# Kernel tuning notes

Measured on AMD Instinct MI355X. Metric: run time of the kernel, lower is better.

The kernel has to match this reference:

```python
import jax, jax.numpy as jnp
import numpy as np

H, K, D = 4096, 16, 256  # hidden_dim, num_slots, slot_dim
BOT = 512                # decoder bottleneck
N_ITER = 3
EPS = 1e-5


def _ln(x, g, b):
    mu = jnp.mean(x, axis=-1, keepdims=True)
    var = jnp.var(x, axis=-1, keepdims=True)
    return (x - mu) * jax.lax.rsqrt(var + EPS) * g + b


def setup_inputs() -> dict:
    key = jax.random.key(0)
    ks = jax.random.split(key, 24)
    r = lambda i, shape, s=0.02: jax.random.normal(ks[i], shape, jnp.float32) * s
    inp = {
        "hidden_states": jax.random.normal(ks[0], (8, 4096, H), jnp.float32),
        "old_slots": jax.random.normal(ks[1], (8, K, D), jnp.float32) * 0.02,
        # SlotAttention params
        "in_w": r(2, (H, D)), "in_b": jnp.zeros((D,), jnp.float32),
        "ln_in_g": jnp.ones((D,), jnp.float32), "ln_in_b": jnp.zeros((D,), jnp.float32),
        "ln_s_g": jnp.ones((D,), jnp.float32), "ln_s_b": jnp.zeros((D,), jnp.float32),
        "ln_m_g": jnp.ones((D,), jnp.float32), "ln_m_b": jnp.zeros((D,), jnp.float32),
        "q_w": r(3, (D, D)), "k_w": r(4, (D, D)), "v_w": r(5, (D, D)),
        "mlp_w1": r(6, (D, 2 * D)), "mlp_b1": jnp.zeros((2 * D,), jnp.float32),
        "mlp_w2": r(7, (2 * D, D)), "mlp_b2": jnp.zeros((D,), jnp.float32),
        # ReconstructionDecoder params
        "dec_w1": r(8, (D, BOT)), "dec_b1": jnp.zeros((BOT,), jnp.float32),
        "dec_w2": r(9, (BOT, BOT)), "dec_b2": jnp.zeros((BOT,), jnp.float32),
        "dec_w3": r(10, (BOT, H)), "dec_b3": jnp.zeros((H,), jnp.float32),
    }
    return inp


def _forward(hidden_states, old_slots, in_w, in_b, ln_in_g, ln_in_b, ln_s_g, ln_s_b,
             ln_m_g, ln_m_b, q_w, k_w, v_w, mlp_w1, mlp_b1, mlp_w2, mlp_b2,
             dec_w1, dec_b1, dec_w2, dec_b2, dec_w3, dec_b3):
    B, T, _ = hidden_states.shape
    # subsample: 256 linspace over front + last 256 tokens (T > 512 branch)
    idx_front = jnp.linspace(0.0, T - 256, 256).astype(jnp.int32)  # torch long cast truncates; values are exact floor here
    idx_back = jnp.arange(T - 256, T, dtype=jnp.int32)
    idx = jnp.concatenate([idx_front, idx_back])
    sampled = hidden_states[:, idx, :]                 # [B, 512, H]

    x = _ln(sampled @ in_w + in_b, ln_in_g, ln_in_b)   # [B, 512, D]
    k = x @ k_w                                        # [B, 512, D]
    v = x @ v_w
    scale = D ** (-0.5)

    slots = old_slots                                  # [B, K, D]
    for _ in range(N_ITER):
        s = _ln(slots, ln_s_g, ln_s_b)
        q = s @ q_w
        logits = jnp.einsum('bkd,bnd->bkn', q, k) * scale
        attn = jax.nn.softmax(logits, axis=1)          # softmax over SLOT axis
        upd = jnp.einsum('bkn,bnd->bkd', attn, v)
        h = _ln(upd, ln_m_g, ln_m_b)
        slots = s + jax.nn.gelu(h @ mlp_w1 + mlp_b1, approximate=False) @ mlp_w2 + mlp_b2

    # reconstruction loss
    target = jax.lax.stop_gradient(jnp.mean(hidden_states, axis=1))     # [B, H]
    r = jax.nn.gelu(slots @ dec_w1 + dec_b1, approximate=False)
    r = jax.nn.gelu(r @ dec_w2 + dec_b2, approximate=False)
    r = r @ dec_w3 + dec_b3                                             # [B, K, H]
    recon = jnp.mean(r, axis=1)                                         # [B, H]
    recon_loss = jnp.mean((recon - target) ** 2)
    return slots, recon_loss


def reference(hidden_states, old_slots, in_w, in_b, ln_in_g, ln_in_b, ln_s_g, ln_s_b,
              ln_m_g, ln_m_b, q_w, k_w, v_w, mlp_w1, mlp_b1, mlp_w2, mlp_b2,
              dec_w1, dec_b1, dec_w2, dec_b2, dec_w3, dec_b3):
    return _forward(hidden_states, old_slots, in_w, in_b, ln_in_g, ln_in_b, ln_s_g,
                    ln_s_b, ln_m_g, ln_m_b, q_w, k_w, v_w, mlp_w1, mlp_b1, mlp_w2,
                    mlp_b2, dec_w1, dec_b1, dec_w2, dec_b2, dec_w3, dec_b3)
```

## Files before the change

kernel.cpp:

```cpp
#include <hip/hip_runtime.h>

typedef unsigned short u16;
typedef float f32x4 __attribute__((ext_vector_type(4)));
typedef __bf16 bf16x8 __attribute__((ext_vector_type(8)));
typedef u16 u16x4 __attribute__((ext_vector_type(4)));

__device__ __forceinline__ u16 f2bf(float f){
  __bf16 h = (__bf16)f;
  union { __bf16 h; u16 u; } x; x.h = h;
  return x.u;
}
__device__ __forceinline__ float bf2f(u16 s){
  union { unsigned u; float f; } x; x.u = ((unsigned)s) << 16;
  return x.f;
}
__device__ __forceinline__ f32x4 mfma16(bf16x8 a, bf16x8 b, f32x4 c){
  return __builtin_amdgcn_mfma_f32_16x16x32_bf16(a, b, c, 0, 0, 0);
}
__device__ __forceinline__ float wred_sum(float x){
  #pragma unroll
  for (int m = 1; m < 64; m <<= 1) x += __shfl_xor(x, m);
  return x;
}
__device__ __forceinline__ float gelu_f(float v){
  return 0.5f * v * (1.0f + erff(v * 0.70710678118654752440f));
}
__device__ __forceinline__ int sample_idx(int r){
  return (r < 256) ? (3840 * r) / 255 : (3584 + r);
}

__global__ __launch_bounds__(256) void k_prep(
    const float* __restrict__ in_w, const float* __restrict__ q_w,
    const float* __restrict__ k_w, const float* __restrict__ v_w,
    const float* __restrict__ w1, const float* __restrict__ w2,
    u16* __restrict__ in_wT, u16* __restrict__ q_wT, u16* __restrict__ k_wT,
    u16* __restrict__ v_wT, u16* __restrict__ w1T, u16* __restrict__ w2T,
    float* __restrict__ loss_slot)
{
  __shared__ float tile[64][65];
  int id = blockIdx.x;
  const float* src; u16* dst; int R, C, t;
  if (id < 256)      { src=in_w; dst=in_wT; R=4096; C=256; t=id; }
  else if (id < 272) { src=q_w;  dst=q_wT;  R=256;  C=256; t=id-256; }
  else if (id < 288) { src=k_w;  dst=k_wT;  R=256;  C=256; t=id-272; }
  else if (id < 304) { src=v_w;  dst=v_wT;  R=256;  C=256; t=id-288; }
  else if (id < 336) { src=w1;   dst=w1T;   R=256;  C=512; t=id-304; }
  else               { src=w2;   dst=w2T;   R=512;  C=256; t=id-336; }
  int tC = C >> 6;
  int r0 = (t / tC) * 64, c0 = (t % tC) * 64;
  int tr = threadIdx.x >> 6, tc = threadIdx.x & 63;
  #pragma unroll
  for (int rr = tr; rr < 64; rr += 4)
    tile[rr][tc] = src[(size_t)(r0+rr)*C + c0 + tc];
  __syncthreads();
  #pragma unroll
  for (int cc = tr; cc < 64; cc += 4)
    dst[(size_t)(c0+cc)*R + r0 + tc] = f2bf(tile[tc][cc]);
  if (id == 0 && threadIdx.x == 0) *loss_slot = 0.f;
}

__global__ __launch_bounds__(256) void k_colsum(const float* __restrict__ hs,
                                                float* __restrict__ parts)
{
  int tc = blockIdx.x;
  int hb = blockIdx.y;
  int b  = blockIdx.z;
  int h0 = hb*1024 + threadIdx.x*4;
  const float* p = hs + ((size_t)b*4096 + (size_t)tc*64)*4096 + h0;
  f32x4 s = {0.f,0.f,0.f,0.f};
  for (int t = 0; t < 64; ++t)
    s += *reinterpret_cast<const f32x4*>(p + (size_t)t*4096);
  *reinterpret_cast<f32x4*>(parts + ((size_t)(b*64+tc) << 12) + h0) = s;
}

__global__ __launch_bounds__(256) void k_colsum2(const float* __restrict__ parts,
                                                 float* __restrict__ tgt)
{
  int i = blockIdx.x*256 + threadIdx.x;
  int b = i >> 12, h = i & 4095;
  float s = 0.f;
  for (int c = 0; c < 64; ++c) s += parts[((size_t)(b*64+c) << 12) + h];
  tgt[i] = s * (1.0f/4096.0f);
}

__global__ __launch_bounds__(512) void k_in_gemm_ln(
    const float* __restrict__ hs, const u16* __restrict__ in_wT,
    const float* __restrict__ in_b,
    const float* __restrict__ ln_g, const float* __restrict__ ln_b,
    u16* __restrict__ x_b)
{
  __shared__ float xt[16][260];
  const int lane = threadIdx.x & 63;
  const int w = threadIdx.x >> 6;
  const int c16 = lane & 15, g4 = lane >> 4;
  const int m0 = blockIdx.x * 16;
  const int row = m0 + c16;
  const int b = row >> 9;
  const int tok = row & 511;
  const int src = sample_idx(tok);
  const float* arow = hs + ((size_t)b*4096 + src)*4096 + g4*8;

  f32x4 acc[2];
  acc[0] = (f32x4){0.f,0.f,0.f,0.f};
  acc[1] = (f32x4){0.f,0.f,0.f,0.f};

  for (int k0 = 0; k0 < 4096; k0 += 32) {
    f32x4 a0 = *reinterpret_cast<const f32x4*>(arow + k0);
    f32x4 a1 = *reinterpret_cast<const f32x4*>(arow + k0 + 4);
    union { u16 u[8]; bf16x8 v; } af;
    #pragma unroll
    for (int i=0;i<4;++i){ af.u[i] = f2bf(a0[i]); af.u[4+i] = f2bf(a1[i]); }
    #pragma unroll
    for (int ct=0; ct<2; ++ct){
      int col = w*32 + ct*16 + c16;
      bf16x8 bf = *reinterpret_cast<const bf16x8*>(in_wT + (size_t)col*4096 + k0 + g4*8);
      acc[ct] = mfma16(af.v, bf, acc[ct]);
    }
  }
  #pragma unroll
  for (int ct=0; ct<2; ++ct){
    int col = w*32 + ct*16 + c16;
    float bias = in_b[col];
    #pragma unroll
    for (int i=0;i<4;++i) xt[g4*4+i][col] = acc[ct][i] + bias;
  }
  __syncthreads();
  #pragma unroll
  for (int rr=0; rr<2; ++rr){
    int r = 2*w + rr;
    f32x4 v = *reinterpret_cast<const f32x4*>(&xt[r][4*lane]);
    float s = v[0]+v[1]+v[2]+v[3];
    float q = v[0]*v[0]+v[1]*v[1]+v[2]*v[2]+v[3]*v[3];
    s = wred_sum(s); q = wred_sum(q);
    float mu = s*(1.0f/256.0f);
    float var = q*(1.0f/256.0f) - mu*mu;
    float rs = rsqrtf(var + 1e-5f);
    u16x4 pk;
    #pragma unroll
    for (int i=0;i<4;++i) pk[i] = f2bf((v[i]-mu)*rs*ln_g[4*lane+i] + ln_b[4*lane+i]);
    *reinterpret_cast<u16x4*>(x_b + (size_t)(m0 + r)*256 + 4*lane) = pk;
  }
}

__global__ __launch_bounds__(256) void k_kv(
    const u16* __restrict__ x_b, const u16* __restrict__ k_wT, const u16* __restrict__ v_wT,
    u16* __restrict__ k_out, u16* __restrict__ vT_out)
{
  const int lane = threadIdx.x & 63;
  const int w = threadIdx.x >> 6;
  const int c16 = lane & 15, g4 = lane >> 4;
  const int m0 = blockIdx.x * 16;
  const u16* aptr = x_b + (size_t)(m0 + c16)*256 + g4*8;
  f32x4 ak[4], av[4];
  #pragma unroll
  for (int ct=0; ct<4; ++ct){ ak[ct]=(f32x4){0.f,0.f,0.f,0.f}; av[ct]=(f32x4){0.f,0.f,0.f,0.f}; }
  #pragma unroll
  for (int kk=0; kk<8; ++kk){
    bf16x8 af = *reinterpret_cast<const bf16x8*>(aptr + kk*32);
    #pragma unroll
    for (int ct=0; ct<4; ++ct){
      int col = w*64 + ct*16 + c16;
      bf16x8 bk = *reinterpret_cast<const bf16x8*>(k_wT + (size_t)col*256 + kk*32 + g4*8);
      bf16x8 bv = *reinterpret_cast<const bf16x8*>(v_wT + (size_t)col*256 + kk*32 + g4*8);
      ak[ct] = mfma16(af, bk, ak[ct]);
      av[ct] = mfma16(af, bv, av[ct]);
    }
  }
  const int b = m0 >> 9;
  const int tok0 = (m0 & 511) + g4*4;
  #pragma unroll
  for (int ct=0; ct<4; ++ct){
    int col = w*64 + ct*16 + c16;
    #pragma unroll
    for (int i=0;i<4;++i)
      k_out[(size_t)(m0 + g4*4 + i)*256 + col] = f2bf(ak[ct][i]);
    u16x4 pk;
    #pragma unroll
    for (int i=0;i<4;++i) pk[i] = f2bf(av[ct][i]);
    *reinterpret_cast<u16x4*>(vT_out + ((size_t)(b*256 + col))*512 + tok0) = pk;
  }
}

__global__ __launch_bounds__(1024) void k_slots(
    const float* __restrict__ old_slots,
    const u16* __restrict__ k_b, const u16* __restrict__ vT_b,
    const u16* __restrict__ q_wT, const u16* __restrict__ w1T, const u16* __restrict__ w2T,
    const float* __restrict__ ln_s_g, const float* __restrict__ ln_s_b,
    const float* __restrict__ ln_m_g, const float* __restrict__ ln_m_b,
    const float* __restrict__ mlp_b1, const float* __restrict__ mlp_b2,
    float* __restrict__ out_slots)
{
  __shared__ u16 bufA[16*264];
  __shared__ u16 qS[16*264];
  __shared__ u16 wideS[16*520];
  __shared__ u16 updS[16*264];

  const int lane = threadIdx.x & 63;
  const int w    = threadIdx.x >> 6;
  const int c16  = lane & 15;
  const int g4   = lane >> 4;
  const int b    = blockIdx.x;

  const u16* kb = k_b  + (size_t)b * 512 * 256;
  const u16* vb = vT_b + (size_t)b * 256 * 512;

  float sl[4];
  {
    const float* p = old_slots + ((size_t)b*16 + w)*256 + 4*lane;
    #pragma unroll
    for (int i=0;i<4;++i) sl[i] = p[i];
  }
  float lsg[4], lsbv[4], lmg[4], lmb[4];
  #pragma unroll
  for (int i=0;i<4;++i){
    lsg[i]  = ln_s_g[4*lane+i];
    lsbv[i] = ln_s_b[4*lane+i];
    lmg[i]  = ln_m_g[4*lane+i];
    lmb[i]  = ln_m_b[4*lane+i];
  }
  const float b1a = mlp_b1[32*w + c16];
  const float b1b = mlp_b1[32*w + 16 + c16];
  const float b2c = mlp_b2[16*w + c16];
  float sv[4];

  for (int it = 0; it < 3; ++it) {
    {
      float s = sl[0]+sl[1]+sl[2]+sl[3];
      float q = sl[0]*sl[0]+sl[1]*sl[1]+sl[2]*sl[2]+sl[3]*sl[3];
      s = wred_sum(s); q = wred_sum(q);
      float mu = s * (1.0f/256.0f);
      float var = q * (1.0f/256.0f) - mu*mu;
      float rs = rsqrtf(var + 1e-5f);
      u16x4 pk;
      #pragma unroll
      for (int i=0;i<4;++i){ sv[i] = (sl[i]-mu)*rs*lsg[i] + lsbv[i]; pk[i] = f2bf(sv[i]); }
      *reinterpret_cast<u16x4*>(bufA + w*264 + 4*lane) = pk;
    }
    __syncthreads();

    {
      f32x4 acc = {0.f,0.f,0.f,0.f};
      #pragma unroll
      for (int kk = 0; kk < 8; ++kk) {
        bf16x8 af = *reinterpret_cast<const bf16x8*>(bufA + c16*264 + kk*32 + g4*8);
        bf16x8 bf = *reinterpret_cast<const bf16x8*>(q_wT + (size_t)(16*w + c16)*256 + kk*32 + g4*8);
        acc = mfma16(af, bf, acc);
      }
      #pragma unroll
      for (int i=0;i<4;++i) qS[(g4*4+i)*264 + 16*w + c16] = f2bf(acc[i]);
    }
    __syncthreads();

    {
      bf16x8 qf[8];
      #pragma unroll
      for (int kk=0;kk<8;++kk)
        qf[kk] = *reinterpret_cast<const bf16x8*>(qS + c16*264 + kk*32 + g4*8);
      #pragma unroll
      for (int ct=0; ct<2; ++ct) {
        int n0 = 32*w + 16*ct;
        f32x4 acc = {0.f,0.f,0.f,0.f};
        #pragma unroll
        for (int kk=0;kk<8;++kk){
          bf16x8 bf = *reinterpret_cast<const bf16x8*>(kb + (size_t)(n0 + c16)*256 + kk*32 + g4*8);
          acc = mfma16(qf[kk], bf, acc);
        }
        float t0 = acc[0]*0.0625f, t1 = acc[1]*0.0625f, t2 = acc[2]*0.0625f, t3 = acc[3]*0.0625f;
        float mx = fmaxf(fmaxf(t0,t1), fmaxf(t2,t3));
        mx = fmaxf(mx, __shfl_xor(mx,16));
        mx = fmaxf(mx, __shfl_xor(mx,32));
        float e0 = expf(t0-mx), e1 = expf(t1-mx), e2 = expf(t2-mx), e3 = expf(t3-mx);
        float ss = e0+e1+e2+e3;
        ss += __shfl_xor(ss,16);
        ss += __shfl_xor(ss,32);
        float inv = 1.0f/ss;
        wideS[(g4*4+0)*520 + n0 + c16] = f2bf(e0*inv);
        wideS[(g4*4+1)*520 + n0 + c16] = f2bf(e1*inv);
        wideS[(g4*4+2)*520 + n0 + c16] = f2bf(e2*inv);
        wideS[(g4*4+3)*520 + n0 + c16] = f2bf(e3*inv);
      }
    }
    __syncthreads();

    {
      f32x4 acc = {0.f,0.f,0.f,0.f};
      #pragma unroll
      for (int kk=0; kk<16; ++kk){
        bf16x8 af = *reinterpret_cast<const bf16x8*>(wideS + c16*520 + kk*32 + g4*8);
        bf16x8 bf = *reinterpret_cast<const bf16x8*>(vb + (size_t)(16*w + c16)*512 + kk*32 + g4*8);
        acc = mfma16(af, bf, acc);
      }
      #pragma unroll
      for (int i=0;i<4;++i) updS[(g4*4+i)*264 + 16*w + c16] = f2bf(acc[i]);
    }
    __syncthreads();

    {
      u16x4 up = *reinterpret_cast<const u16x4*>(updS + w*264 + 4*lane);
      float uv[4];
      #pragma unroll
      for (int i=0;i<4;++i) uv[i] = bf2f(up[i]);
      float s = uv[0]+uv[1]+uv[2]+uv[3];
      float q = uv[0]*uv[0]+uv[1]*uv[1]+uv[2]*uv[2]+uv[3]*uv[3];
      s = wred_sum(s); q = wred_sum(q);
      float mu = s*(1.0f/256.0f);
      float var = q*(1.0f/256.0f) - mu*mu;
      float rs = rsqrtf(var + 1e-5f);
      u16x4 pk;
      #pragma unroll
      for (int i=0;i<4;++i) pk[i] = f2bf((uv[i]-mu)*rs*lmg[i] + lmb[i]);
      *reinterpret_cast<u16x4*>(bufA + w*264 + 4*lane) = pk;
    }
    __syncthreads();

    {
      bf16x8 hf[8];
      #pragma unroll
      for (int kk=0;kk<8;++kk)
        hf[kk] = *reinterpret_cast<const bf16x8*>(bufA + c16*264 + kk*32 + g4*8);
      #pragma unroll
      for (int ct=0; ct<2; ++ct){
        int n0 = 32*w + 16*ct;
        float bb = ct ? b1b : b1a;
        f32x4 acc = {0.f,0.f,0.f,0.f};
        #pragma unroll
        for (int kk=0;kk<8;++kk){
          bf16x8 bf = *reinterpret_cast<const bf16x8*>(w1T + (size_t)(n0 + c16)*256 + kk*32 + g4*8);
          acc = mfma16(hf[kk], bf, acc);
        }
        #pragma unroll
        for (int i=0;i<4;++i)
          wideS[(g4*4+i)*520 + n0 + c16] = f2bf(gelu_f(acc[i] + bb));
      }
    }
    __syncthreads();

    {
      f32x4 acc = {0.f,0.f,0.f,0.f};
      #pragma unroll
      for (int kk=0; kk<16; ++kk){
        bf16x8 af = *reinterpret_cast<const bf16x8*>(wideS + c16*520 + kk*32 + g4*8);
        bf16x8 bf = *reinterpret_cast<const bf16x8*>(w2T + (size_t)(16*w + c16)*512 + kk*32 + g4*8);
        acc = mfma16(af, bf, acc);
      }
      #pragma unroll
      for (int i=0;i<4;++i) bufA[(g4*4+i)*264 + 16*w + c16] = f2bf(acc[i] + b2c);
    }
    __syncthreads();
    {
      u16x4 ns = *reinterpret_cast<const u16x4*>(bufA + w*264 + 4*lane);
      #pragma unroll
      for (int i=0;i<4;++i) sl[i] = sv[i] + bf2f(ns[i]);
    }
    __syncthreads();
  }

  {
    float* p = out_slots + ((size_t)b*16 + w)*256 + 4*lane;
    #pragma unroll
    for (int i=0;i<4;++i) p[i] = sl[i];
  }
}

__global__ __launch_bounds__(256) void k_dec(
    const float* __restrict__ slots, const float* __restrict__ w1, const float* __restrict__ b1,
    const float* __restrict__ w2, const float* __restrict__ b2, float* __restrict__ r2g)
{
  __shared__ float sr[256];
  __shared__ float r1[512];
  const int row = blockIdx.x;
  const int t = threadIdx.x;
  sr[t] = slots[(size_t)row*256 + t];
  __syncthreads();
  float a0 = b1[t], a1 = b1[t+256];
  for (int i=0;i<256;++i){
    float s = sr[i];
    a0 = fmaf(s, w1[(size_t)i*512 + t], a0);
    a1 = fmaf(s, w1[(size_t)i*512 + t + 256], a1);
  }
  r1[t] = gelu_f(a0); r1[t+256] = gelu_f(a1);
  __syncthreads();
  float c0 = b2[t], c1 = b2[t+256];
  for (int i=0;i<512;++i){
    float s = r1[i];
    c0 = fmaf(s, w2[(size_t)i*512 + t], c0);
    c1 = fmaf(s, w2[(size_t)i*512 + t + 256], c1);
  }
  r2g[(size_t)row*512 + t]       = gelu_f(c0);
  r2g[(size_t)row*512 + t + 256] = gelu_f(c1);
}

__global__ __launch_bounds__(256) void k_loss_part(
    const float* __restrict__ r2g, const float* __restrict__ w3, const float* __restrict__ b3,
    float* __restrict__ rpart)
{
  __shared__ float rb[128];
  const int hb = blockIdx.x;
  const int b  = blockIdx.y;
  const int jc = blockIdx.z;
  const int t  = threadIdx.x;
  const int j0 = jc*128;
  if (t < 128){
    float s = 0.f;
    #pragma unroll
    for (int k2=0;k2<16;++k2) s += r2g[(size_t)(b*16 + k2)*512 + j0 + t];
    rb[t] = s * (1.0f/16.0f);
  }
  __syncthreads();
  const int h = hb*1024 + t*4;
  f32x4 acc;
  if (jc == 0) acc = *reinterpret_cast<const f32x4*>(b3 + h);
  else         acc = (f32x4){0.f,0.f,0.f,0.f};
  for (int j=0;j<128;++j){
    f32x4 wv = *reinterpret_cast<const f32x4*>(w3 + (size_t)(j0+j)*4096 + h);
    float rj = rb[j];
    acc[0] = fmaf(rj, wv[0], acc[0]);
    acc[1] = fmaf(rj, wv[1], acc[1]);
    acc[2] = fmaf(rj, wv[2], acc[2]);
    acc[3] = fmaf(rj, wv[3], acc[3]);
  }
  *reinterpret_cast<f32x4*>(rpart + (((size_t)jc*8 + b) << 12) + h) = acc;
}

__global__ __launch_bounds__(256) void k_loss_final(
    const float* __restrict__ rpart, const float* __restrict__ tgt,
    float* __restrict__ loss)
{
  __shared__ float red[4];
  int i = blockIdx.x*256 + threadIdx.x;
  int b = i >> 12, h = i & 4095;
  float r = 0.f;
  #pragma unroll
  for (int jc=0; jc<4; ++jc) r += rpart[(((size_t)jc*8 + b) << 12) + h];
  float d = r - tgt[i];
  float loc = wred_sum(d*d);
  const int lane = threadIdx.x & 63, wv_ = threadIdx.x >> 6;
  if (lane == 0) red[wv_] = loc;
  __syncthreads();
  if (threadIdx.x == 0){
    float s = (red[0]+red[1]+red[2]+red[3]) * (1.0f/32768.0f);
    atomicAdd(loss, s);
  }
}

extern "C" void kernel_launch(void* const* d_in, const int* in_sizes, int n_in,
                              void* d_out, int out_size, void* d_ws, size_t ws_size,
                              hipStream_t stream)
{
  const float* hs      = (const float*)d_in[0];
  const float* oslots  = (const float*)d_in[1];
  const float* in_w    = (const float*)d_in[2];
  const float* in_b    = (const float*)d_in[3];
  const float* ln_in_g = (const float*)d_in[4];
  const float* ln_in_b = (const float*)d_in[5];
  const float* ln_s_g  = (const float*)d_in[6];
  const float* ln_s_b  = (const float*)d_in[7];
  const float* ln_m_g  = (const float*)d_in[8];
  const float* ln_m_b  = (const float*)d_in[9];
  const float* q_w     = (const float*)d_in[10];
  const float* k_w     = (const float*)d_in[11];
  const float* v_w     = (const float*)d_in[12];
  const float* mlp_w1  = (const float*)d_in[13];
  const float* mlp_b1  = (const float*)d_in[14];
  const float* mlp_w2  = (const float*)d_in[15];
  const float* mlp_b2  = (const float*)d_in[16];
  const float* dec_w1  = (const float*)d_in[17];
  const float* dec_b1  = (const float*)d_in[18];
  const float* dec_w2  = (const float*)d_in[19];
  const float* dec_b2  = (const float*)d_in[20];
  const float* dec_w3  = (const float*)d_in[21];
  const float* dec_b3  = (const float*)d_in[22];

  char* ws = (char*)d_ws;
  size_t off = 0;
  auto alloc = [&](size_t bytes)->char*{
    char* p = ws + off; off = (off + bytes + 255) & ~(size_t)255; return p;
  };
  float* tgt   = (float*)alloc((size_t)32768*4);
  float* parts = (float*)alloc((size_t)8*64*4096*4);
  u16* in_wT = (u16*)alloc((size_t)256*4096*2);
  u16* q_wT  = (u16*)alloc((size_t)65536*2);
  u16* k_wT  = (u16*)alloc((size_t)65536*2);
  u16* v_wT  = (u16*)alloc((size_t)65536*2);
  u16* w1T   = (u16*)alloc((size_t)131072*2);
  u16* w2T   = (u16*)alloc((size_t)131072*2);
  u16* x_b   = (u16*)alloc((size_t)4096*256*2);
  u16* kk_b  = (u16*)alloc((size_t)4096*256*2);
  u16* vT_b  = (u16*)alloc((size_t)8*256*512*2);
  float* r2g = (float*)alloc((size_t)128*512*4);
  float* rpart = (float*)alloc((size_t)4*8*4096*4);

  float* out_slots = (float*)d_out;
  float* out_loss  = out_slots + 32768;

  hipLaunchKernelGGL(k_prep, dim3(368), dim3(256), 0, stream,
      in_w, q_w, k_w, v_w, mlp_w1, mlp_w2, in_wT, q_wT, k_wT, v_wT, w1T, w2T, out_loss);
  hipLaunchKernelGGL(k_colsum, dim3(64,4,8), dim3(256), 0, stream, hs, parts);
  hipLaunchKernelGGL(k_colsum2, dim3(128), dim3(256), 0, stream, parts, tgt);
  hipLaunchKernelGGL(k_in_gemm_ln, dim3(256), dim3(512), 0, stream,
      hs, in_wT, in_b, ln_in_g, ln_in_b, x_b);
  hipLaunchKernelGGL(k_kv, dim3(256), dim3(256), 0, stream, x_b, k_wT, v_wT, kk_b, vT_b);
  hipLaunchKernelGGL(k_slots, dim3(8), dim3(1024), 0, stream,
      oslots, kk_b, vT_b, q_wT, w1T, w2T,
      ln_s_g, ln_s_b, ln_m_g, ln_m_b, mlp_b1, mlp_b2, out_slots);
  hipLaunchKernelGGL(k_dec, dim3(128), dim3(256), 0, stream,
      out_slots, dec_w1, dec_b1, dec_w2, dec_b2, r2g);
  hipLaunchKernelGGL(k_loss_part, dim3(4,8,4), dim3(256), 0, stream,
      r2g, dec_w3, dec_b3, rpart);
  hipLaunchKernelGGL(k_loss_final, dim3(128), dim3(256), 0, stream,
      rpart, tgt, out_loss);
}
```

Before: 1.086 ms.

## Widen input GEMM to 1024 threads, batch decoder loss GEMM, fuse target reduction

The input projection kernel now runs 16 waves per block, each computing one 16-column tile with an unrolled K loop instead of two tiles per wave. This spreads the strided, latency-bound fp32 row loads across more waves. The reconstruction loss kernel is restructured so each block handles all 8 batches for a 64-wide slice of the bottleneck. Each w3 element is then loaded once and reused across batches instead of once per batch. The separate column-sum finalize kernel is dropped, and its reduction is folded into the loss-final kernel, which saves a launch but makes that kernel read 64 partials per output.

```diff
diff --git a/kernel.cpp b/kernel.cpp
--- a/kernel.cpp
+++ b/kernel.cpp
@@ -1,6 +1,7 @@
 #include <hip/hip_runtime.h>
 
 typedef unsigned short u16;
+typedef float f32x2 __attribute__((ext_vector_type(2)));
 typedef float f32x4 __attribute__((ext_vector_type(4)));
 typedef __bf16 bf16x8 __attribute__((ext_vector_type(8)));
 typedef u16 u16x4 __attribute__((ext_vector_type(4)));
@@ -73,17 +74,7 @@
   *reinterpret_cast<f32x4*>(parts + ((size_t)(b*64+tc) << 12) + h0) = s;
 }
 
-__global__ __launch_bounds__(256) void k_colsum2(const float* __restrict__ parts,
-                                                 float* __restrict__ tgt)
-{
-  int i = blockIdx.x*256 + threadIdx.x;
-  int b = i >> 12, h = i & 4095;
-  float s = 0.f;
-  for (int c = 0; c < 64; ++c) s += parts[((size_t)(b*64+c) << 12) + h];
-  tgt[i] = s * (1.0f/4096.0f);
-}
-
-__global__ __launch_bounds__(512) void k_in_gemm_ln(
+__global__ __launch_bounds__(1024) void k_in_gemm_ln(
     const float* __restrict__ hs, const u16* __restrict__ in_wT,
     const float* __restrict__ in_b,
     const float* __restrict__ ln_g, const float* __restrict__ ln_b,
@@ -99,35 +90,29 @@
   const int tok = row & 511;
   const int src = sample_idx(tok);
   const float* arow = hs + ((size_t)b*4096 + src)*4096 + g4*8;
-
-  f32x4 acc[2];
-  acc[0] = (f32x4){0.f,0.f,0.f,0.f};
-  acc[1] = (f32x4){0.f,0.f,0.f,0.f};
-
+  const u16* bcol = in_wT + (size_t)(w*16 + c16)*4096 + g4*8;
+
+  f32x4 acc = {0.f,0.f,0.f,0.f};
+
+  #pragma unroll 4
   for (int k0 = 0; k0 < 4096; k0 += 32) {
     f32x4 a0 = *reinterpret_cast<const f32x4*>(arow + k0);
     f32x4 a1 = *reinterpret_cast<const f32x4*>(arow + k0 + 4);
+    bf16x8 bf = *reinterpret_cast<const bf16x8*>(bcol + k0);
     union { u16 u[8]; bf16x8 v; } af;
     #pragma unroll
     for (int i=0;i<4;++i){ af.u[i] = f2bf(a0[i]); af.u[4+i] = f2bf(a1[i]); }
-    #pragma unroll
-    for (int ct=0; ct<2; ++ct){
-      int col = w*32 + ct*16 + c16;
-      bf16x8 bf = *reinterpret_cast<const bf16x8*>(in_wT + (size_t)col*4096 + k0 + g4*8);
-      acc[ct] = mfma16(af.v, bf, acc[ct]);
-    }
-  }
-  #pragma unroll
-  for (int ct=0; ct<2; ++ct){
-    int col = w*32 + ct*16 + c16;
+    acc = mfma16(af.v, bf, acc);
+  }
+  {
+    int col = w*16 + c16;
     float bias = in_b[col];
     #pragma unroll
-    for (int i=0;i<4;++i) xt[g4*4+i][col] = acc[ct][i] + bias;
+    for (int i=0;i<4;++i) xt[g4*4+i][col] = acc[i] + bias;
   }
   __syncthreads();
-  #pragma unroll
-  for (int rr=0; rr<2; ++rr){
-    int r = 2*w + rr;
+  {
+    int r = w;
     f32x4 v = *reinterpret_cast<const f32x4*>(&xt[r][4*lane]);
     float s = v[0]+v[1]+v[2]+v[3];
     float q = v[0]*v[0]+v[1]*v[1]+v[2]*v[2]+v[3]*v[3];
@@ -394,45 +379,58 @@
     const float* __restrict__ r2g, const float* __restrict__ w3, const float* __restrict__ b3,
     float* __restrict__ rpart)
 {
-  __shared__ float rb[128];
-  const int hb = blockIdx.x;
-  const int b  = blockIdx.y;
-  const int jc = blockIdx.z;
+  __shared__ float rb[8][64];
+  const int jc = blockIdx.x;
+  const int hb = blockIdx.y;
   const int t  = threadIdx.x;
-  const int j0 = jc*128;
-  if (t < 128){
+  const int j0 = jc*64;
+  #pragma unroll
+  for (int e = t; e < 512; e += 256){
+    int b = e >> 6, jj = e & 63;
     float s = 0.f;
     #pragma unroll
-    for (int k2=0;k2<16;++k2) s += r2g[(size_t)(b*16 + k2)*512 + j0 + t];
-    rb[t] = s * (1.0f/16.0f);
+    for (int k2=0;k2<16;++k2) s += r2g[(size_t)(b*16 + k2)*512 + j0 + jj];
+    rb[b][jj] = s * (1.0f/16.0f);
   }
   __syncthreads();
-  const int h = hb*1024 + t*4;
-  f32x4 acc;
-  if (jc == 0) acc = *reinterpret_cast<const f32x4*>(b3 + h);
-  else         acc = (f32x4){0.f,0.f,0.f,0.f};
-  for (int j=0;j<128;++j){
-    f32x4 wv = *reinterpret_cast<const f32x4*>(w3 + (size_t)(j0+j)*4096 + h);
-    float rj = rb[j];
-    acc[0] = fmaf(rj, wv[0], acc[0]);
-    acc[1] = fmaf(rj, wv[1], acc[1]);
-    acc[2] = fmaf(rj, wv[2], acc[2]);
-    acc[3] = fmaf(rj, wv[3], acc[3]);
-  }
-  *reinterpret_cast<f32x4*>(rpart + (((size_t)jc*8 + b) << 12) + h) = acc;
+  const int h = hb*512 + t*2;
+  f32x2 acc[8];
+  if (jc == 0){
+    f32x2 bv = *reinterpret_cast<const f32x2*>(b3 + h);
+    #pragma unroll
+    for (int b=0;b<8;++b) acc[b] = bv;
+  } else {
+    #pragma unroll
+    for (int b=0;b<8;++b) acc[b] = (f32x2){0.f,0.f};
+  }
+  for (int j=0;j<64;++j){
+    f32x2 wv = *reinterpret_cast<const f32x2*>(w3 + (size_t)(j0+j)*4096 + h);
+    #pragma unroll
+    for (int b=0;b<8;++b){
+      float rj = rb[b][j];
+      acc[b][0] = fmaf(rj, wv[0], acc[b][0]);
+      acc[b][1] = fmaf(rj, wv[1], acc[b][1]);
+    }
+  }
+  #pragma unroll
+  for (int b=0;b<8;++b)
+    *reinterpret_cast<f32x2*>(rpart + (((size_t)jc*8 + b) << 12) + h) = acc[b];
 }
 
 __global__ __launch_bounds__(256) void k_loss_final(
-    const float* __restrict__ rpart, const float* __restrict__ tgt,
+    const float* __restrict__ rpart, const float* __restrict__ parts,
     float* __restrict__ loss)
 {
   __shared__ float red[4];
   int i = blockIdx.x*256 + threadIdx.x;
   int b = i >> 12, h = i & 4095;
+  float tg = 0.f;
+  for (int c = 0; c < 64; ++c) tg += parts[((size_t)(b*64+c) << 12) + h];
+  tg *= (1.0f/4096.0f);
   float r = 0.f;
   #pragma unroll
-  for (int jc=0; jc<4; ++jc) r += rpart[(((size_t)jc*8 + b) << 12) + h];
-  float d = r - tgt[i];
+  for (int jc=0; jc<8; ++jc) r += rpart[(((size_t)jc*8 + b) << 12) + h];
+  float d = r - tg;
   float loc = wred_sum(d*d);
   const int lane = threadIdx.x & 63, wv_ = threadIdx.x >> 6;
   if (lane == 0) red[wv_] = loc;
@@ -476,7 +474,6 @@
   auto alloc = [&](size_t bytes)->char*{
     char* p = ws + off; off = (off + bytes + 255) & ~(size_t)255; return p;
   };
-  float* tgt   = (float*)alloc((size_t)32768*4);
   float* parts = (float*)alloc((size_t)8*64*4096*4);
   u16* in_wT = (u16*)alloc((size_t)256*4096*2);
   u16* q_wT  = (u16*)alloc((size_t)65536*2);
@@ -488,7 +485,7 @@
   u16* kk_b  = (u16*)alloc((size_t)4096*256*2);
   u16* vT_b  = (u16*)alloc((size_t)8*256*512*2);
   float* r2g = (float*)alloc((size_t)128*512*4);
-  float* rpart = (float*)alloc((size_t)4*8*4096*4);
+  float* rpart = (float*)alloc((size_t)64*4096*4);
 
   float* out_slots = (float*)d_out;
   float* out_loss  = out_slots + 32768;
@@ -496,8 +493,7 @@
   hipLaunchKernelGGL(k_prep, dim3(368), dim3(256), 0, stream,
       in_w, q_w, k_w, v_w, mlp_w1, mlp_w2, in_wT, q_wT, k_wT, v_wT, w1T, w2T, out_loss);
   hipLaunchKernelGGL(k_colsum, dim3(64,4,8), dim3(256), 0, stream, hs, parts);
-  hipLaunchKernelGGL(k_colsum2, dim3(128), dim3(256), 0, stream, parts, tgt);
-  hipLaunchKernelGGL(k_in_gemm_ln, dim3(256), dim3(512), 0, stream,
+  hipLaunchKernelGGL(k_in_gemm_ln, dim3(256), dim3(1024), 0, stream,
       hs, in_wT, in_b, ln_in_g, ln_in_b, x_b);
   hipLaunchKernelGGL(k_kv, dim3(256), dim3(256), 0, stream, x_b, k_wT, v_wT, kk_b, vT_b);
   hipLaunchKernelGGL(k_slots, dim3(8), dim3(1024), 0, stream,
@@ -505,8 +501,8 @@
       ln_s_g, ln_s_b, ln_m_g, ln_m_b, mlp_b1, mlp_b2, out_slots);
   hipLaunchKernelGGL(k_dec, dim3(128), dim3(256), 0, stream,
       out_slots, dec_w1, dec_b1, dec_w2, dec_b2, r2g);
-  hipLaunchKernelGGL(k_loss_part, dim3(4,8,4), dim3(256), 0, stream,
+  hipLaunchKernelGGL(k_loss_part, dim3(8,8), dim3(256), 0, stream,
       r2g, dec_w3, dec_b3, rpart);
   hipLaunchKernelGGL(k_loss_final, dim3(128), dim3(256), 0, stream,
-      rpart, tgt, out_loss);
-}
+      rpart, parts, out_loss);
+}
```

Measured after the change: 1.137 ms. +4.7%, slower.
